# Kernel tuning notes

Measured on AMD Instinct MI355X. Metric: run time of the kernel, lower is better.

Reference implementation:

```python
import jax, jax.numpy as jnp
import numpy as np

D_MODEL = 1024
N_HEADS = 16
D_HEAD = 64
INIT_RANGE = 0.02
IGNORE = -100000.0


def setup_inputs() -> dict:
    key = jax.random.key(0)
    ks = jax.random.split(key, 5)
    x = jax.random.normal(ks[0], (2, 2048, D_MODEL), dtype=jnp.float32)
    W_Q = jax.random.normal(ks[1], (N_HEADS, D_MODEL, D_HEAD), dtype=jnp.float32) * INIT_RANGE
    W_K = jax.random.normal(ks[2], (N_HEADS, D_MODEL, D_HEAD), dtype=jnp.float32) * INIT_RANGE
    W_V = jax.random.normal(ks[3], (N_HEADS, D_MODEL, D_HEAD), dtype=jnp.float32) * INIT_RANGE
    W_O = jax.random.normal(ks[4], (N_HEADS, D_HEAD, D_MODEL), dtype=jnp.float32) * INIT_RANGE
    b_Q = jnp.zeros((N_HEADS, D_HEAD), dtype=jnp.float32)
    b_K = jnp.zeros((N_HEADS, D_HEAD), dtype=jnp.float32)
    b_V = jnp.zeros((N_HEADS, D_HEAD), dtype=jnp.float32)
    b_O = jnp.zeros((D_MODEL,), dtype=jnp.float32)
    return {"normalized_resid_pre": x, "W_Q": W_Q, "W_K": W_K, "W_V": W_V,
            "W_O": W_O, "b_Q": b_Q, "b_K": b_K, "b_V": b_V, "b_O": b_O}


def reference(normalized_resid_pre, W_Q, W_K, W_V, W_O, b_Q, b_K, b_V, b_O):
    x = normalized_resid_pre  # [b, s, d_model]
    q = jnp.einsum('bsd,hde->bshe', x, W_Q) + b_Q  # [b, s, h, d_head]
    k = jnp.einsum('bsd,hde->bshe', x, W_K) + b_K
    v = jnp.einsum('bsd,hde->bshe', x, W_V) + b_V
    scores = jnp.einsum('bqhe,bkhe->bhqk', q, k) / jnp.sqrt(jnp.float32(D_HEAD))
    s = x.shape[1]
    causal = jnp.arange(s)[:, None] >= jnp.arange(s)[None, :]  # [q, k]
    scores = jnp.where(causal, scores, jnp.float32(IGNORE))
    pattern = jax.nn.softmax(scores, axis=-1)  # [b, h, q, k]
    z = jnp.einsum('bkhe,bhqk->bqhe', v, pattern)
    out = jnp.einsum('bqhe,hed->bqd', z, W_O) + b_O
    return out
```

## Files before the change

### kernel.cpp

```cpp
#include <hip/hip_runtime.h>

#define SEQ 2048
#define BATCH 2
#define DM 1024
#define NH 16
#define DH 64

typedef __bf16 bf16;
typedef __bf16 bf16x8 __attribute__((ext_vector_type(8)));
typedef __bf16 bf16x4 __attribute__((ext_vector_type(4)));
typedef float f32x4 __attribute__((ext_vector_type(4)));

#define MFMA16(a, b, c) __builtin_amdgcn_mfma_f32_16x16x32_bf16((a), (b), (c), 0, 0, 0)

#if __has_builtin(__builtin_amdgcn_exp2f)
#define EXP2(x) __builtin_amdgcn_exp2f(x)
#else
#define EXP2(x) exp2f(x)
#endif

#define QSCALE 0.18033688f

typedef __attribute__((address_space(3))) void lds_void;
typedef __attribute__((address_space(1))) void glb_void;
__device__ __forceinline__ void gld16(void* lds, const void* g) {
    __builtin_amdgcn_global_load_lds((const glb_void*)g, (lds_void*)lds, 16, 0, 0);
}

__global__ __launch_bounds__(256) void k_prep(const float* __restrict__ x,
                                              const float* __restrict__ WQ,
                                              const float* __restrict__ WK,
                                              const float* __restrict__ WV,
                                              const float* __restrict__ WO,
                                              bf16* __restrict__ xb,
                                              bf16* __restrict__ wT,
                                              bf16* __restrict__ woT) {
    int bx = blockIdx.x;
    int t = threadIdx.x;
    if (bx < 2048) {
        int g = bx * 256 + t;
        const float4* x4 = (const float4*)x;
        float4 a = x4[2 * g];
        float4 b = x4[2 * g + 1];
        bf16x8 o;
        o[0] = (bf16)a.x; o[1] = (bf16)a.y; o[2] = (bf16)a.z; o[3] = (bf16)a.w;
        o[4] = (bf16)b.x; o[5] = (bf16)b.y; o[6] = (bf16)b.z; o[7] = (bf16)b.w;
        *(bf16x8*)(xb + 8 * g) = o;
        return;
    }
    __shared__ bf16 T[64 * 65];
    if (bx < 2816) {
        int id = bx - 2048;
        int kt = id & 15, ph = id >> 4;
        int p = ph >> 4, h = ph & 15;
        const float* Wp = (p == 0) ? WQ : (p == 1) ? WK : WV;
        const float* src = Wp + ((size_t)h * DM + (size_t)kt * 64) * DH;
        for (int i = 0; i < 4; i++) {
            int c = t + 256 * i;
            int r = c >> 4;
            int col = (c & 15) * 4;
            float4 v = *(const float4*)&src[r * 64 + col];
            T[(col + 0) * 65 + r] = (bf16)v.x;
            T[(col + 1) * 65 + r] = (bf16)v.y;
            T[(col + 2) * 65 + r] = (bf16)v.z;
            T[(col + 3) * 65 + r] = (bf16)v.w;
        }
        __syncthreads();
        bf16* dst = wT + (size_t)ph * 64 * DM + (size_t)kt * 64;
        for (int i = 0; i < 2; i++) {
            int c = t + 256 * i;
            int e = c >> 3;
            int k0 = (c & 7) * 8;
            bf16x8 o;
            for (int j = 0; j < 8; j++) o[j] = T[e * 65 + k0 + j];
            *(bf16x8*)&dst[(size_t)e * DM + k0] = o;
        }
    } else {
        int id = bx - 2816;
        int ht = id & 15, dt = id >> 4;
        for (int i = 0; i < 4; i++) {
            int c = t + 256 * i;
            int r = c >> 4;
            int col = (c & 15) * 4;
            float4 v = *(const float4*)&WO[((size_t)(ht * 64 + r)) * DM + dt * 64 + col];
            T[(col + 0) * 65 + r] = (bf16)v.x;
            T[(col + 1) * 65 + r] = (bf16)v.y;
            T[(col + 2) * 65 + r] = (bf16)v.z;
            T[(col + 3) * 65 + r] = (bf16)v.w;
        }
        __syncthreads();
        for (int i = 0; i < 2; i++) {
            int c = t + 256 * i;
            int d = c >> 3;
            int h0 = (c & 7) * 8;
            bf16x8 o;
            for (int j = 0; j < 8; j++) o[j] = T[d * 65 + h0 + j];
            *(bf16x8*)&woT[((size_t)(dt * 64 + d)) * DM + ht * 64 + h0] = o;
        }
    }
}

__global__ __launch_bounds__(256, 3) void k_qkv(const bf16* __restrict__ xb,
                                                const bf16* __restrict__ wT,
                                                const float* __restrict__ bQ,
                                                const float* __restrict__ bK,
                                                const float* __restrict__ bV,
                                                bf16* __restrict__ Qb,
                                                bf16* __restrict__ Kb,
                                                bf16* __restrict__ VTf) {
    int mt = blockIdx.x, nt = blockIdx.y, p = blockIdx.z;
    __shared__ __align__(16) bf16 Ws[2][16 * 512];
    int t = threadIdx.x;
    int lane = t & 63, w = t >> 6;
    int l15 = lane & 15, quad = lane >> 4;

    const f32x4 z4 = {0.f, 0.f, 0.f, 0.f};
    f32x4 acc[2][8];
    for (int mi = 0; mi < 2; mi++)
        for (int ni = 0; ni < 8; ni++) acc[mi][ni] = z4;

    int m0 = mt * 128, n0 = nt * 128;
    int kl = quad * 8;
    const bf16* a0p = xb + (size_t)(m0 + w * 32 + l15) * DM + kl;
    const bf16* a1p = a0p + (size_t)16 * DM;
    const bf16* wrow = wT + ((size_t)p * 1024 + n0) * DM;

    auto stageW = [&](int buf, int k0) {
#pragma unroll
        for (int i = 0; i < 4; i++) {
            int f = w + 4 * i;
            int ks = f >> 3, ni = f & 7;
            gld16(&Ws[buf][f * 512],
                  wrow + (size_t)(ni * 16 + l15) * DM + k0 + ks * 32 + quad * 8);
        }
    };

    bf16x8 xr[2][2][2];
    stageW(0, 0);
#pragma unroll
    for (int ks = 0; ks < 2; ks++) {
        xr[0][0][ks] = *(const bf16x8*)(a0p + ks * 32);
        xr[0][1][ks] = *(const bf16x8*)(a1p + ks * 32);
    }

#pragma unroll
    for (int it = 0; it < 16; it++) {
        int buf = it & 1;
        __syncthreads();
        if (it < 15) {
            int kn = (it + 1) * 64;
            stageW(buf ^ 1, kn);
#pragma unroll
            for (int ks = 0; ks < 2; ks++) {
                xr[buf ^ 1][0][ks] = *(const bf16x8*)(a0p + kn + ks * 32);
                xr[buf ^ 1][1][ks] = *(const bf16x8*)(a1p + kn + ks * 32);
            }
        }
#pragma unroll
        for (int ks = 0; ks < 2; ks++) {
#pragma unroll
            for (int ni = 0; ni < 8; ni++) {
                bf16x8 bfr = *(const bf16x8*)&Ws[buf][(ks * 8 + ni) * 512 + lane * 8];
                acc[0][ni] = MFMA16(xr[buf][0][ks], bfr, acc[0][ni]);
                acc[1][ni] = MFMA16(xr[buf][1][ks], bfr, acc[1][ni]);
            }
        }
    }

    int b = mt >> 4;
    int kt = mt & 15;
    int s00 = kt * 128;
    if (p < 2) {
        const float* bias = (p == 0) ? bQ : bK;
        bf16* dst = (p == 0) ? Qb : Kb;
        float scale = (p == 0) ? QSCALE : 1.0f;
        for (int ni = 0; ni < 8; ni++) {
            int he = n0 + ni * 16 + l15;
            int h = he >> 6, e = he & 63;
            float bia = bias[he];
            size_t rb = (size_t)(b * NH + h) * SEQ * DH + e;
            for (int mi = 0; mi < 2; mi++)
                for (int r = 0; r < 4; r++) {
                    int s = s00 + w * 32 + mi * 16 + quad * 4 + r;
                    dst[rb + (size_t)s * DH] = (bf16)((acc[mi][ni][r] + bia) * scale);
                }
        }
    } else {
        for (int ni = 0; ni < 8; ni++) {
            int he = n0 + ni * 16 + l15;
            int h = he >> 6, e = he & 63;
            int no = (e >> 4) & 3;
            float bia = bV[he];
            size_t base = (((size_t)(b * NH + h) * 16 + kt) * 16 + (w * 4 + no)) * 512
                          + (size_t)((quad << 4) | l15) * 8;
            for (int mi = 0; mi < 2; mi++) {
                bf16x4 o;
                for (int r = 0; r < 4; r++) o[r] = (bf16)(acc[mi][ni][r] + bia);
                *(bf16x4*)&VTf[base + mi * 4] = o;
            }
        }
    }
}

__global__ __launch_bounds__(512, 4) void k_attn(const bf16* __restrict__ Qb,
                                                 const bf16* __restrict__ Kb,
                                                 const bf16* __restrict__ VTf,
                                                 bf16* __restrict__ Zb) {
    int bh = blockIdx.x;
    int y = blockIdx.y;
    int qt = (y < 8) ? y : 23 - y;
    int h = bh & 15, b = bh >> 4;
    __shared__ __align__(16) bf16 Ks[2][16 * 512];
    __shared__ __align__(16) bf16 Vs[16 * 512];
    int t = threadIdx.x;
    int lane = t & 63, w = t >> 6;
    int l15 = lane & 15, quad = lane >> 4;

    const bf16* qbase = Qb + (size_t)bh * SEQ * DH;
    const bf16* kbase = Kb + (size_t)bh * SEQ * DH;
    const bf16* vfrag = VTf + (size_t)bh * 16 * 8192;

    int qr0 = qt * 128 + w * 16;
    bf16x8 aq[2];
    for (int ks = 0; ks < 2; ks++)
        aq[ks] = *(const bf16x8*)&qbase[(size_t)(qr0 + l15) * DH + ks * 32 + quad * 8];

    auto stageK = [&](int buf, int kt) {
        for (int i = 0; i < 2; i++) {
            int f = w * 2 + i;
            int ks = f >> 3, ni = f & 7;
            gld16(&Ks[buf][f * 512],
                  kbase + (size_t)(kt * 128 + ni * 16 + l15) * DH + ks * 32 + quad * 8);
        }
    };
    auto stageV = [&](int kt) {
        const bf16* vt = vfrag + (size_t)kt * 8192;
        for (int i = 0; i < 2; i++) {
            int f = w * 2 + i;
            gld16(&Vs[f * 512], vt + f * 512 + lane * 8);
        }
    };

    const bf16 one = (bf16)1.0f;
    const bf16x8 ones = {one, one, one, one, one, one, one, one};
    const f32x4 z4 = {0.f, 0.f, 0.f, 0.f};
    f32x4 acco[4], accd;
    for (int no = 0; no < 4; no++) acco[no] = z4;
    accd = z4;

    stageK(0, 0);

    for (int kt = 0; kt <= qt; kt++) {
        int buf = kt & 1;
        __syncthreads();
        stageV(kt);
        if (kt < qt) stageK(buf ^ 1, kt + 1);
        const bf16* Kbuf = Ks[buf];

        f32x4 accs[8];
        for (int ni = 0; ni < 8; ni++) accs[ni] = z4;
        for (int ks = 0; ks < 2; ks++)
            for (int ni = 0; ni < 8; ni++) {
                bf16x8 ak = *(const bf16x8*)&Kbuf[(ks * 8 + ni) * 512 + lane * 8];
                accs[ni] = MFMA16(ak, aq[ks], accs[ni]);
            }

        if (kt == qt) {
            int ql = w * 16 + l15;
            for (int ni = 0; ni < 8; ni++) {
                int kvl = ni * 16 + quad * 4;
                for (int r = 0; r < 4; r++)
                    if (kvl + r > ql) accs[ni][r] = -1e30f;
            }
        }

        bf16x4 pt[8];
        for (int ni = 0; ni < 8; ni++)
            for (int r = 0; r < 4; r++)
                pt[ni][r] = (bf16)EXP2(accs[ni][r]);

        __syncthreads();

        for (int p4 = 0; p4 < 4; p4++) {
            bf16x8 ap;
            for (int j = 0; j < 4; j++) {
                ap[j] = pt[2 * p4][j];
                ap[4 + j] = pt[2 * p4 + 1][j];
            }
            accd = MFMA16(ap, ones, accd);
            for (int no = 0; no < 4; no++) {
                bf16x8 bv = *(const bf16x8*)&Vs[(p4 * 4 + no) * 512 + lane * 8];
                acco[no] = MFMA16(ap, bv, acco[no]);
            }
        }
    }

    for (int r = 0; r < 4; r++) {
        float inv = 1.0f / accd[r];
        int q = qr0 + quad * 4 + r;
        size_t rowbase = ((size_t)b * SEQ + q) * DM + h * DH;
        for (int no = 0; no < 4; no++)
            Zb[rowbase + no * 16 + l15] = (bf16)(acco[no][r] * inv);
    }
}

__global__ __launch_bounds__(256, 4) void k_out(const bf16* __restrict__ Zb,
                                                const bf16* __restrict__ woT,
                                                const float* __restrict__ bO,
                                                float* __restrict__ out) {
    int mt = blockIdx.x;
    int nt = blockIdx.y;
    __shared__ __align__(16) bf16 Ws[2][8 * 512];
    int t = threadIdx.x;
    int lane = t & 63, w = t >> 6;
    int l15 = lane & 15, quad = lane >> 4;

    int m0 = mt * 128, n0 = nt * 64;
    int kl = quad * 8;
    const bf16* a0p = Zb + (size_t)(m0 + w * 32 + l15) * DM + kl;
    const bf16* a1p = a0p + (size_t)16 * DM;
    const bf16* wrow = woT + (size_t)n0 * DM;

    const f32x4 z4 = {0.f, 0.f, 0.f, 0.f};
    f32x4 acc[2][4];
    for (int mi = 0; mi < 2; mi++)
        for (int ni = 0; ni < 4; ni++) acc[mi][ni] = z4;

    auto stageW = [&](int buf, int k0) {
#pragma unroll
        for (int i = 0; i < 2; i++) {
            int f = w * 2 + i;
            int ks = f >> 2, ni = f & 3;
            gld16(&Ws[buf][f * 512],
                  wrow + (size_t)(ni * 16 + l15) * DM + k0 + ks * 32 + quad * 8);
        }
    };

    bf16x8 xr[2][2][2];
    stageW(0, 0);
#pragma unroll
    for (int ks = 0; ks < 2; ks++) {
        xr[0][0][ks] = *(const bf16x8*)(a0p + ks * 32);
        xr[0][1][ks] = *(const bf16x8*)(a1p + ks * 32);
    }

#pragma unroll
    for (int it = 0; it < 16; it++) {
        int buf = it & 1;
        __syncthreads();
        if (it < 15) {
            int kn = (it + 1) * 64;
            stageW(buf ^ 1, kn);
#pragma unroll
            for (int ks = 0; ks < 2; ks++) {
                xr[buf ^ 1][0][ks] = *(const bf16x8*)(a0p + kn + ks * 32);
                xr[buf ^ 1][1][ks] = *(const bf16x8*)(a1p + kn + ks * 32);
            }
        }
#pragma unroll
        for (int ks = 0; ks < 2; ks++) {
#pragma unroll
            for (int ni = 0; ni < 4; ni++) {
                bf16x8 bfr = *(const bf16x8*)&Ws[buf][(ks * 4 + ni) * 512 + lane * 8];
                acc[0][ni] = MFMA16(xr[buf][0][ks], bfr, acc[0][ni]);
                acc[1][ni] = MFMA16(xr[buf][1][ks], bfr, acc[1][ni]);
            }
        }
    }
    for (int ni = 0; ni < 4; ni++) {
        int d = n0 + ni * 16 + l15;
        float bia = bO[d];
        for (int mi = 0; mi < 2; mi++)
            for (int r = 0; r < 4; r++) {
                int s = m0 + w * 32 + mi * 16 + quad * 4 + r;
                out[(size_t)s * DM + d] = acc[mi][ni][r] + bia;
            }
    }
}

extern "C" void kernel_launch(void* const* d_in, const int* in_sizes, int n_in,
                              void* d_out, int out_size, void* d_ws, size_t ws_size,
                              hipStream_t stream) {
    const float* x  = (const float*)d_in[0];
    const float* WQ = (const float*)d_in[1];
    const float* WK = (const float*)d_in[2];
    const float* WV = (const float*)d_in[3];
    const float* WO = (const float*)d_in[4];
    const float* bQ = (const float*)d_in[5];
    const float* bK = (const float*)d_in[6];
    const float* bV = (const float*)d_in[7];
    const float* bO = (const float*)d_in[8];
    float* out = (float*)d_out;

    char* w = (char*)d_ws;
    bf16* xb    = (bf16*)(w + 0);
    bf16* wqkvT = (bf16*)(w + (8u << 20));
    bf16* woT   = (bf16*)(w + (14u << 20));
    bf16* Qb    = (bf16*)(w + (16u << 20));
    bf16* Kb    = (bf16*)(w + (24u << 20));
    bf16* VTf   = (bf16*)(w + (32u << 20));
    bf16* Zb    = (bf16*)(w + (40u << 20));

    k_prep<<<3072, 256, 0, stream>>>(x, WQ, WK, WV, WO, xb, wqkvT, woT);
    k_qkv<<<dim3(32, 8, 3), 256, 0, stream>>>(xb, wqkvT, bQ, bK, bV, Qb, Kb, VTf);
    k_attn<<<dim3(32, 16), 512, 0, stream>>>(Qb, Kb, VTf, Zb);
    k_out<<<dim3(32, 16), 256, 0, stream>>>(Zb, woT, bO, out);
}
```

Before: 194.7 us.

## Restructure QKV GEMM into 256x256 tiles with 4-stage swizzled LDS pipeline

The QKV projection GEMM now uses 256x256 output tiles with 8 waves per block. Both A (activations) and B (weights) are staged through LDS in a 4-deep ring of XOR-swizzled buffers, with explicit vmcnt waits and raw s_barrier calls. MFMA runs are split into two half-steps with raised wave priority, interleaved with the next prefetches. The larger tiles cut global re-reads of x and the weights, but the grid shrinks to 192 blocks, which may underfill the GPU's CUs, and each block needs 128KB of LDS.

Result: faster. 179.1 us (-8.0%).

```diff
diff --git a/kernel.cpp b/kernel.cpp
--- a/kernel.cpp
+++ b/kernel.cpp
@@ -100,7 +100,7 @@
     }
 }
 
-__global__ __launch_bounds__(256, 3) void k_qkv(const bf16* __restrict__ xb,
+__global__ __launch_bounds__(512, 2) void k_qkv(const bf16* __restrict__ xb,
                                                 const bf16* __restrict__ wT,
                                                 const float* __restrict__ bQ,
                                                 const float* __restrict__ bK,
@@ -109,94 +109,140 @@
                                                 bf16* __restrict__ Kb,
                                                 bf16* __restrict__ VTf) {
     int mt = blockIdx.x, nt = blockIdx.y, p = blockIdx.z;
-    __shared__ __align__(16) bf16 Ws[2][16 * 512];
+    __shared__ __align__(16) char sm[131072];
     int t = threadIdx.x;
     int lane = t & 63, w = t >> 6;
     int l15 = lane & 15, quad = lane >> 4;
+    int wr = w >> 2, wc = w & 3;
+    int m0 = mt * 256, n0 = nt * 256;
+
+    int P0 = t * 16;
+    int L0 = P0 ^ (((P0 >> 7) & 3) << 4);
+    int row0 = L0 >> 6, kc0 = (L0 >> 4) & 3;
+    int P1 = 8192 + t * 16;
+    int L1 = P1 ^ (((P1 >> 7) & 3) << 4);
+    int row1 = L1 >> 6, kc1 = (L1 >> 4) & 3;
+    const bf16* gA0 = xb + (size_t)(m0 + row0) * DM + kc0 * 8;
+    const bf16* gA1 = xb + (size_t)(m0 + row1) * DM + kc1 * 8;
+    const bf16* gB0 = wT + (size_t)(p * 1024 + n0 + row0) * DM + kc0 * 8;
+    const bf16* gB1 = wT + (size_t)(p * 1024 + n0 + row1) * DM + kc1 * 8;
+
+    auto stage = [&](int ts, bool bsel) {
+        char* sb = sm + (ts & 3) * 32768;
+        int ko = ts * 32;
+        if (!bsel) {
+            gld16(sb + w * 1024, gA0 + ko);
+            gld16(sb + 8192 + w * 1024, gA1 + ko);
+        } else {
+            gld16(sb + 16384 + w * 1024, gB0 + ko);
+            gld16(sb + 16384 + 8192 + w * 1024, gB1 + ko);
+        }
+    };
+
+    int aoff[8], boff[4];
+#pragma unroll
+    for (int mi = 0; mi < 8; mi++) {
+        int row = wr * 128 + mi * 16 + l15;
+        aoff[mi] = row * 64 + ((quad ^ ((row >> 1) & 3)) << 4);
+    }
+#pragma unroll
+    for (int ni = 0; ni < 4; ni++) {
+        int row = wc * 64 + ni * 16 + l15;
+        boff[ni] = 16384 + row * 64 + ((quad ^ ((row >> 1) & 3)) << 4);
+    }
 
     const f32x4 z4 = {0.f, 0.f, 0.f, 0.f};
-    f32x4 acc[2][8];
-    for (int mi = 0; mi < 2; mi++)
-        for (int ni = 0; ni < 8; ni++) acc[mi][ni] = z4;
-
-    int m0 = mt * 128, n0 = nt * 128;
-    int kl = quad * 8;
-    const bf16* a0p = xb + (size_t)(m0 + w * 32 + l15) * DM + kl;
-    const bf16* a1p = a0p + (size_t)16 * DM;
-    const bf16* wrow = wT + ((size_t)p * 1024 + n0) * DM;
-
-    auto stageW = [&](int buf, int k0) {
-#pragma unroll
-        for (int i = 0; i < 4; i++) {
-            int f = w + 4 * i;
-            int ks = f >> 3, ni = f & 7;
-            gld16(&Ws[buf][f * 512],
-                  wrow + (size_t)(ni * 16 + l15) * DM + k0 + ks * 32 + quad * 8);
-        }
+    f32x4 acc[8][4];
+#pragma unroll
+    for (int mi = 0; mi < 8; mi++)
+#pragma unroll
+        for (int ni = 0; ni < 4; ni++) acc[mi][ni] = z4;
+
+    auto kstep = [&](int tt, bool st) {
+        const char* sb = sm + (tt & 3) * 32768;
+        bf16x8 bfr[4], afr[4];
+#pragma unroll
+        for (int ni = 0; ni < 4; ni++) bfr[ni] = *(const bf16x8*)(sb + boff[ni]);
+#pragma unroll
+        for (int mi = 0; mi < 4; mi++) afr[mi] = *(const bf16x8*)(sb + aoff[mi]);
+        if (st) stage(tt + 3, false);
+        __builtin_amdgcn_s_setprio(1);
+#pragma unroll
+        for (int mi = 0; mi < 4; mi++)
+#pragma unroll
+            for (int ni = 0; ni < 4; ni++)
+                acc[mi][ni] = MFMA16(afr[mi], bfr[ni], acc[mi][ni]);
+        __builtin_amdgcn_s_setprio(0);
+        asm volatile("s_barrier" ::: "memory");
+        bf16x8 afr2[4];
+#pragma unroll
+        for (int mi = 0; mi < 4; mi++) afr2[mi] = *(const bf16x8*)(sb + aoff[4 + mi]);
+        if (st) stage(tt + 3, true);
+        __builtin_amdgcn_s_setprio(1);
+#pragma unroll
+        for (int mi = 0; mi < 4; mi++)
+#pragma unroll
+            for (int ni = 0; ni < 4; ni++)
+                acc[4 + mi][ni] = MFMA16(afr2[mi], bfr[ni], acc[4 + mi][ni]);
+        __builtin_amdgcn_s_setprio(0);
     };
 
-    bf16x8 xr[2][2][2];
-    stageW(0, 0);
-#pragma unroll
-    for (int ks = 0; ks < 2; ks++) {
-        xr[0][0][ks] = *(const bf16x8*)(a0p + ks * 32);
-        xr[0][1][ks] = *(const bf16x8*)(a1p + ks * 32);
-    }
-
-#pragma unroll
-    for (int it = 0; it < 16; it++) {
-        int buf = it & 1;
-        __syncthreads();
-        if (it < 15) {
-            int kn = (it + 1) * 64;
-            stageW(buf ^ 1, kn);
-#pragma unroll
-            for (int ks = 0; ks < 2; ks++) {
-                xr[buf ^ 1][0][ks] = *(const bf16x8*)(a0p + kn + ks * 32);
-                xr[buf ^ 1][1][ks] = *(const bf16x8*)(a1p + kn + ks * 32);
-            }
-        }
-#pragma unroll
-        for (int ks = 0; ks < 2; ks++) {
-#pragma unroll
-            for (int ni = 0; ni < 8; ni++) {
-                bf16x8 bfr = *(const bf16x8*)&Ws[buf][(ks * 8 + ni) * 512 + lane * 8];
-                acc[0][ni] = MFMA16(xr[buf][0][ks], bfr, acc[0][ni]);
-                acc[1][ni] = MFMA16(xr[buf][1][ks], bfr, acc[1][ni]);
-            }
-        }
-    }
-
-    int b = mt >> 4;
-    int kt = mt & 15;
-    int s00 = kt * 128;
+    stage(0, false); stage(0, true);
+    stage(1, false); stage(1, true);
+    stage(2, false); stage(2, true);
+
+#pragma unroll 1
+    for (int tt = 0; tt < 29; tt++) {
+        asm volatile("s_waitcnt vmcnt(8)\n\ts_barrier" ::: "memory");
+        __builtin_amdgcn_sched_barrier(0);
+        kstep(tt, true);
+    }
+    asm volatile("s_waitcnt vmcnt(8)\n\ts_barrier" ::: "memory");
+    __builtin_amdgcn_sched_barrier(0);
+    kstep(29, false);
+    asm volatile("s_waitcnt vmcnt(4)\n\ts_barrier" ::: "memory");
+    __builtin_amdgcn_sched_barrier(0);
+    kstep(30, false);
+    asm volatile("s_waitcnt vmcnt(0)\n\ts_barrier" ::: "memory");
+    __builtin_amdgcn_sched_barrier(0);
+    kstep(31, false);
+
+    int b = m0 >> 11;
     if (p < 2) {
         const float* bias = (p == 0) ? bQ : bK;
         bf16* dst = (p == 0) ? Qb : Kb;
         float scale = (p == 0) ? QSCALE : 1.0f;
-        for (int ni = 0; ni < 8; ni++) {
-            int he = n0 + ni * 16 + l15;
+#pragma unroll
+        for (int ni = 0; ni < 4; ni++) {
+            int he = n0 + wc * 64 + ni * 16 + l15;
             int h = he >> 6, e = he & 63;
             float bia = bias[he];
             size_t rb = (size_t)(b * NH + h) * SEQ * DH + e;
-            for (int mi = 0; mi < 2; mi++)
+#pragma unroll
+            for (int mi = 0; mi < 8; mi++)
+#pragma unroll
                 for (int r = 0; r < 4; r++) {
-                    int s = s00 + w * 32 + mi * 16 + quad * 4 + r;
+                    int s = ((m0 + wr * 128 + mi * 16 + quad * 4 + r) & 2047);
                     dst[rb + (size_t)s * DH] = (bf16)((acc[mi][ni][r] + bia) * scale);
                 }
         }
     } else {
-        for (int ni = 0; ni < 8; ni++) {
-            int he = n0 + ni * 16 + l15;
-            int h = he >> 6, e = he & 63;
-            int no = (e >> 4) & 3;
+#pragma unroll
+        for (int ni = 0; ni < 4; ni++) {
+            int he = n0 + wc * 64 + ni * 16 + l15;
+            int h = he >> 6;
             float bia = bV[he];
-            size_t base = (((size_t)(b * NH + h) * 16 + kt) * 16 + (w * 4 + no)) * 512
-                          + (size_t)((quad << 4) | l15) * 8;
-            for (int mi = 0; mi < 2; mi++) {
+#pragma unroll
+            for (int mi = 0; mi < 8; mi++) {
+                int kvl = (mt & 7) * 256 + wr * 128 + mi * 16;
+                int kt = kvl >> 7;
+                int f = (mi >> 1) * 4 + ni;
+                size_t base = (((size_t)(b * NH + h) * 16 + kt) * 16 + f) * 512
+                              + (size_t)((quad << 4) | l15) * 8 + (mi & 1) * 4;
                 bf16x4 o;
+#pragma unroll
                 for (int r = 0; r < 4; r++) o[r] = (bf16)(acc[mi][ni][r] + bia);
-                *(bf16x4*)&VTf[base + mi * 4] = o;
+                *(bf16x4*)&VTf[base] = o;
             }
         }
     }
@@ -402,7 +448,7 @@
     bf16* Zb    = (bf16*)(w + (40u << 20));
 
     k_prep<<<3072, 256, 0, stream>>>(x, WQ, WK, WV, WO, xb, wqkvT, woT);
-    k_qkv<<<dim3(32, 8, 3), 256, 0, stream>>>(xb, wqkvT, bQ, bK, bV, Qb, Kb, VTf);
+    k_qkv<<<dim3(16, 4, 3), 512, 0, stream>>>(xb, wqkvT, bQ, bK, bV, Qb, Kb, VTf);
     k_attn<<<dim3(32, 16), 512, 0, stream>>>(Qb, Kb, VTf, Zb);
     k_out<<<dim3(32, 16), 256, 0, stream>>>(Zb, woT, bO, out);
 }
```
